# Kernel tuning notes

Hardware: AMD Instinct MI355X
Metric: run time of the kernel (lower is better)

## Reference

```python
import jax, jax.numpy as jnp
import numpy as np


def _update_cv(features, labels, ave, cov, amount, class_num):
    # Segment-reduce formulation of the onehot-expand update_CV.
    N, A = features.shape
    C = class_num
    counts = jax.ops.segment_sum(jnp.ones((N,), features.dtype), labels, num_segments=C)  # [C]
    sums = jax.ops.segment_sum(features, labels, num_segments=C)  # [C, A]
    denom = jnp.where(counts == 0, 1.0, counts)[:, None]  # Amount_CxA with zeros -> 1
    ave_CxA = sums / denom
    # var_temp: sum over samples of (x - mean_label)^2, divided by count
    diff = features - ave_CxA[labels]  # [N, A]
    sq = jax.ops.segment_sum(diff * diff, labels, num_segments=C)
    var_temp = sq / denom
    sum_weight = counts[:, None]  # [C,1] broadcast over A
    weight_CV = sum_weight / (sum_weight + amount[:, None])
    weight_CV = jnp.nan_to_num(weight_CV, nan=0.0)
    additional_CV = weight_CV * (1 - weight_CV) * (ave - ave_CxA) ** 2
    new_cov = cov * (1 - weight_CV) + var_temp * weight_CV + additional_CV
    new_ave = ave * (1 - weight_CV) + ave_CxA * weight_CV
    new_amount = amount + counts
    return new_ave, new_cov, new_amount


def _isda_aug(fc_weight, y, labels, cv_matrix, ratio):
    # sigma2[n,c] = ratio * sum_a (W[c,a] - W[labels[n],a])^2 * CV[labels[n],a]
    # = ratio * ( (W^2) @ cv_n - 2 W @ (w_n * cv_n) + sum_a w_n^2 cv_n )
    cv_n = cv_matrix[labels]              # [N, A]
    w_n = fc_weight[labels]               # [N, A]
    t1 = cv_n @ (fc_weight ** 2).T        # [N, C]
    t2 = (w_n * cv_n) @ fc_weight.T       # [N, C]
    t3 = jnp.sum(w_n * w_n * cv_n, axis=1, keepdims=True)  # [N, 1]
    sigma2 = ratio * (t1 - 2.0 * t2 + t3)
    return y + 0.5 * sigma2


def setup_inputs() -> dict:
    key = jax.random.key(0)
    k1, k2, k3, k4 = jax.random.split(key, 4)
    N, A, C = 512, 2048, 1000
    features = jax.random.normal(k1, (N, A), dtype=jnp.float32)
    labels = jax.random.randint(k2, (N,), 0, C)
    fc_weight = jax.random.normal(k3, (C, A), dtype=jnp.float32) * 0.02
    fc_bias = jax.random.normal(k4, (C,), dtype=jnp.float32) * 0.02
    return {
        "features": features,
        "labels": labels,
        "fc_weight": fc_weight,
        "fc_bias": fc_bias,
        "ave_state": jnp.zeros((C, A), jnp.float32),
        "cov_state": jnp.zeros((C, A), jnp.float32),
        "amount_state": jnp.zeros((C,), jnp.float32),
        "ratio": 1,
    }


def reference(features, labels, fc_weight, fc_bias, ave_state, cov_state, amount_state, ratio):
    C = fc_weight.shape[0]
    # model head: y = features @ W^T + b (features come from backbone; detached for CV)
    y = features @ fc_weight.T + fc_bias
    new_ave, new_cov, new_amount = _update_cv(
        jax.lax.stop_gradient(features), labels, ave_state, cov_state, amount_state, C)
    isda_y = _isda_aug(fc_weight, y, labels, jax.lax.stop_gradient(new_cov), ratio)
    log_probs = jax.nn.log_softmax(isda_y, axis=1)
    loss = -jnp.mean(jnp.take_along_axis(log_probs, labels[:, None], axis=1))
    return loss, y, new_ave, new_cov, new_amount
```

## Files before the change

kernel.cpp:

```cpp
#include <hip/hip_runtime.h>
#include <hip/hip_bf16.h>

typedef short v8s __attribute__((ext_vector_type(8)));
typedef float v4f __attribute__((ext_vector_type(4)));

#define KSPLIT 4

static __device__ __forceinline__ float ldv(const void* p, size_t i, int f32m) {
    if (f32m) return ((const float*)p)[i];
    return __bfloat162float(((const __hip_bfloat16*)p)[i]);
}
static __device__ __forceinline__ void stv(void* p, size_t i, float v, int f32m) {
    if (f32m) ((float*)p)[i] = v;
    else ((__hip_bfloat16*)p)[i] = __float2bfloat16(v);
}
static __device__ __forceinline__ unsigned short f2bu(float x) {
    __hip_bfloat16 h = __float2bfloat16(x);
    return *(unsigned short*)&h;
}
static __device__ __forceinline__ float bu2f(unsigned short u) {
    return __uint_as_float(((unsigned)u) << 16);
}

static __device__ __forceinline__ float decode_scalar(const void* p) {
    unsigned u = *(const unsigned*)p;
    unsigned e32 = (u >> 23) & 0xff;
    if (e32 >= 97 && e32 <= 160) return __uint_as_float(u);
    unsigned lo = u & 0xffffu;
    unsigned e16 = (lo >> 7) & 0xff;
    if ((u >> 16) == 0 && e16 >= 97 && e16 <= 160)
        return __uint_as_float(lo << 16);
    return (float)(int)u;
}

static __device__ __forceinline__ int block_sniff(const void* feat) {
    const __hip_bfloat16* p = (const __hip_bfloat16*)feat;
    float v = __bfloat162float(p[threadIdx.x & 255]);
    int bad = !(fabsf(v) < 1e10f);
    return __syncthreads_or(bad) ? 1 : 0;
}

__device__ __forceinline__ float wave_sum(float v) {
    #pragma unroll
    for (int o = 32; o > 0; o >>= 1) v += __shfl_down(v, o, 64);
    return v;
}
__device__ __forceinline__ float wave_max(float v) {
    #pragma unroll
    for (int o = 32; o > 0; o >>= 1) v = fmaxf(v, __shfl_down(v, o, 64));
    return v;
}

static __device__ __forceinline__ void ld16(unsigned short* lds, const unsigned short* g) {
    __builtin_amdgcn_global_load_lds(
        (const __attribute__((address_space(1))) unsigned int*)g,
        (__attribute__((address_space(3))) unsigned int*)lds,
        16, 0, 0);
}

__global__ __launch_bounds__(1024) void count_sort(
        const int* __restrict__ labels, int* __restrict__ counts,
        int* __restrict__ offs, int* __restrict__ rows, int Nn, int C) {
    __shared__ int h[1024];
    __shared__ int o[1024];
    __shared__ int cur[1024];
    int tid = threadIdx.x;
    h[tid] = 0;
    __syncthreads();
    for (int i = tid; i < Nn; i += 1024) atomicAdd(&h[labels[i]], 1);
    __syncthreads();
    o[tid] = h[tid];
    __syncthreads();
    for (int d = 1; d < 1024; d <<= 1) {
        int v = (tid >= d) ? o[tid - d] : 0;
        __syncthreads();
        o[tid] += v;
        __syncthreads();
    }
    int excl = o[tid] - h[tid];
    counts[tid] = h[tid];
    offs[tid] = excl;
    cur[tid] = excl;
    __syncthreads();
    for (int i = tid; i < Nn; i += 1024) {
        int pos = atomicAdd(&cur[labels[i]], 1);
        rows[pos] = i;
    }
}

__global__ __launch_bounds__(256) void prep(
        const void* __restrict__ feat, unsigned short* __restrict__ featb, int total) {
    int f32m = block_sniff(feat);
    int i = (blockIdx.x * 256 + threadIdx.x) * 8;
    if (i >= total) return;
    if (f32m) {
        const float* f = (const float*)feat + i;
        unsigned short r[8];
        #pragma unroll
        for (int u = 0; u < 8; ++u) r[u] = f2bu(f[u]);
        *(v8s*)(featb + i) = *(v8s*)r;
    } else {
        *(v8s*)(featb + i) = *(const v8s*)((const unsigned short*)feat + i);
    }
}

__global__ __launch_bounds__(256) void finalize_stats(
        const unsigned short* __restrict__ featb,
        const int* __restrict__ counts, const int* __restrict__ offs,
        const int* __restrict__ rows,
        const void* __restrict__ ave, const void* __restrict__ cov,
        const void* __restrict__ amount, const void* __restrict__ W,
        const void* __restrict__ feat,
        void* __restrict__ out, size_t off_ave, size_t off_cov, size_t off_amt,
        unsigned short* __restrict__ Wb, unsigned short* __restrict__ W2b,
        unsigned short* __restrict__ Cb, unsigned short* __restrict__ Gb,
        float* __restrict__ T3p, int A, int A8) {
    __shared__ float sb[4];
    int f32m = block_sniff(feat);
    int c = blockIdx.y;
    int a = blockIdx.x * 256 + threadIdx.x;
    size_t idx = (size_t)c * A + a;
    int cnti = counts[c];
    int start = offs[c];
    float s1 = 0.f, s2 = 0.f;
    for (int i = 0; i < cnti; ++i) {
        float x = bu2f(featb[(size_t)rows[start + i] * A + a]);
        s1 += x;
        s2 += x * x;
    }
    float cnt = (float)cnti;
    float denom = cnti > 0 ? cnt : 1.f;
    float mean = s1 / denom;
    float var = fmaxf((s2 - cnt * mean * mean) / denom, 0.f);
    float amt = ldv(amount, c, f32m);
    float tot = cnt + amt;
    float w = tot > 0.f ? (cnt / tot) : 0.f;
    float av = ldv(ave, idx, f32m);
    float cv = ldv(cov, idx, f32m);
    float d = av - mean;
    float ncv = cv * (1.f - w) + var * w + w * (1.f - w) * d * d;
    float nav = av * (1.f - w) + mean * w;
    stv(out, off_cov + idx, ncv, f32m);
    stv(out, off_ave + idx, nav, f32m);
    float wv = ldv(W, idx, f32m);
    Wb[idx] = f2bu(wv);
    W2b[idx] = f2bu(wv * wv);
    Cb[idx] = f2bu(ncv);
    Gb[idx] = f2bu(ncv * wv);
    if (a == 0) stv(out, off_amt + c, amt + cnt, f32m);
    float s = wave_sum(wv * wv * ncv);
    int lane = threadIdx.x & 63, wid = threadIdx.x >> 6;
    if (lane == 0) sb[wid] = s;
    __syncthreads();
    if (threadIdx.x == 0) T3p[(size_t)c * A8 + blockIdx.x] = sb[0] + sb[1] + sb[2] + sb[3];
}

__global__ __launch_bounds__(256) void triple_gemm_mfma(
        const unsigned short* __restrict__ featb,
        const unsigned short* __restrict__ Wb,
        const unsigned short* __restrict__ W2b,
        const unsigned short* __restrict__ Cb,
        const unsigned short* __restrict__ Gb,
        const int* __restrict__ labels,
        float* __restrict__ partY, float* __restrict__ partT1, float* __restrict__ partT2,
        int Cpad, int A, size_t NC) {
    __shared__ unsigned short sA[10240];
    __shared__ int sLab[64];
    int tid = threadIdx.x, wv = tid >> 6, lane = tid & 63;
    int n0 = blockIdx.y * 64, j0 = blockIdx.x * 64;
    int kslice = A / KSPLIT;
    int k0 = blockIdx.z * kslice;
    if (tid < 64) sLab[tid] = labels[n0 + tid];
    __syncthreads();

    int r = lane & 15, q = lane >> 4;
    int fr = wv * 16 + r;
    const unsigned short* pF = featb + (size_t)(n0 + fr) * A + k0 + q * 8;
    int lab = sLab[fr];
    const unsigned short* pC = Cb + (size_t)lab * A + k0 + q * 8;
    const unsigned short* pG = Gb + (size_t)lab * A + k0 + q * 8;
    const unsigned short* pW = Wb + (size_t)(j0 + fr) * A + k0 + q * 8;
    const unsigned short* pQ = W2b + (size_t)(j0 + fr) * A + k0 + q * 8;
    unsigned short* dF = &sA[0    + wv * 512];
    unsigned short* dC = &sA[2048 + wv * 512];
    unsigned short* dG = &sA[4096 + wv * 512];
    unsigned short* dW = &sA[6144 + wv * 512];
    unsigned short* dQ = &sA[8192 + wv * 512];

    v4f aY[4] = {{0,0,0,0},{0,0,0,0},{0,0,0,0},{0,0,0,0}};
    v4f aT1[4] = {{0,0,0,0},{0,0,0,0},{0,0,0,0},{0,0,0,0}};
    v4f aT2[4] = {{0,0,0,0},{0,0,0,0},{0,0,0,0},{0,0,0,0}};

    for (int kk = 0; kk < kslice; kk += 32) {
        ld16(dF, pF); ld16(dC, pC); ld16(dG, pG); ld16(dW, pW); ld16(dQ, pQ);
        pF += 32; pC += 32; pG += 32; pW += 32; pQ += 32;
        __syncthreads();
        v8s f = *(v8s*)&sA[0    + wv * 512 + lane * 8];
        v8s c = *(v8s*)&sA[2048 + wv * 512 + lane * 8];
        v8s g = *(v8s*)&sA[4096 + wv * 512 + lane * 8];
        #pragma unroll
        for (int t = 0; t < 4; ++t) {
            v8s w  = *(v8s*)&sA[6144 + t * 512 + lane * 8];
            v8s w2 = *(v8s*)&sA[8192 + t * 512 + lane * 8];
            aY[t]  = __builtin_amdgcn_mfma_f32_16x16x32_bf16(f, w,  aY[t],  0, 0, 0);
            aT1[t] = __builtin_amdgcn_mfma_f32_16x16x32_bf16(c, w2, aT1[t], 0, 0, 0);
            aT2[t] = __builtin_amdgcn_mfma_f32_16x16x32_bf16(g, w,  aT2[t], 0, 0, 0);
        }
        __syncthreads();
    }

    float* pY = partY + (size_t)blockIdx.z * NC;
    float* p1 = partT1 + (size_t)blockIdx.z * NC;
    float* p2 = partT2 + (size_t)blockIdx.z * NC;
    int quad = lane >> 4, colb = lane & 15;
    #pragma unroll
    for (int t = 0; t < 4; ++t) {
        int j = j0 + t * 16 + colb;
        #pragma unroll
        for (int rr = 0; rr < 4; ++rr) {
            int n = n0 + wv * 16 + quad * 4 + rr;
            size_t idx = (size_t)n * Cpad + j;
            pY[idx] = aY[t][rr];
            p1[idx] = aT1[t][rr];
            p2[idx] = aT2[t][rr];
        }
    }
}

__global__ __launch_bounds__(256) void epilogue_rowloss(
        const float* __restrict__ partY, const float* __restrict__ partT1,
        const float* __restrict__ partT2, const float* __restrict__ T3p,
        const void* __restrict__ bias, const void* __restrict__ feat,
        const int* __restrict__ labels,
        void* __restrict__ out, size_t off_y,
        float* __restrict__ rowloss,
        int C, int Cpad, int A8, const void* ratio_p, size_t NC) {
    __shared__ float sb[4];
    __shared__ float sM;
    __shared__ float sLabVal;
    int f32m = block_sniff(feat);
    int tid = threadIdx.x;
    int n = blockIdx.x;
    int lab = labels[n];
    float t3 = 0.f;
    for (int i = 0; i < A8; ++i) t3 += T3p[(size_t)lab * A8 + i];
    float ratio = decode_scalar(ratio_p);

    float vals[8];
    int nu = Cpad >> 8;
    float m = -3.4e38f;
    for (int u = 0; u < nu; ++u) {
        int j = u * 256 + tid;
        float v = -3.4e38f;
        if (j < C) {
            size_t idx = (size_t)n * Cpad + j;
            float y = 0.f, t1 = 0.f, t2 = 0.f;
            #pragma unroll
            for (int z = 0; z < KSPLIT; ++z) {
                y  += partY[z * NC + idx];
                t1 += partT1[z * NC + idx];
                t2 += partT2[z * NC + idx];
            }
            y += ldv(bias, j, f32m);
            stv(out, off_y + (size_t)n * C + j, y, f32m);
            v = y + 0.5f * ratio * (t1 - 2.f * t2 + t3);
            if (j == lab) sLabVal = v;
        }
        vals[u] = v;
        m = fmaxf(m, v);
    }
    m = wave_max(m);
    int lane = tid & 63, wid = tid >> 6;
    if (lane == 0) sb[wid] = m;
    __syncthreads();
    if (tid == 0) sM = fmaxf(fmaxf(sb[0], sb[1]), fmaxf(sb[2], sb[3]));
    __syncthreads();
    m = sM;
    float s = 0.f;
    for (int u = 0; u < nu; ++u) s += expf(vals[u] - m);
    __syncthreads();
    s = wave_sum(s);
    if (lane == 0) sb[wid] = s;
    __syncthreads();
    if (tid == 0)
        rowloss[n] = m + logf(sb[0] + sb[1] + sb[2] + sb[3]) - sLabVal;
}

__global__ __launch_bounds__(256) void final_loss(
        const float* __restrict__ rowloss, void* __restrict__ out,
        const void* __restrict__ feat, int Nn) {
    __shared__ float sb[4];
    int f32m = block_sniff(feat);
    float s = 0.f;
    for (int i = threadIdx.x; i < Nn; i += 256) s += rowloss[i];
    s = wave_sum(s);
    int lane = threadIdx.x & 63, wid = threadIdx.x >> 6;
    if (lane == 0) sb[wid] = s;
    __syncthreads();
    if (threadIdx.x == 0)
        stv(out, 0, (sb[0] + sb[1] + sb[2] + sb[3]) / (float)Nn, f32m);
}

extern "C" void kernel_launch(void* const* d_in, const int* in_sizes, int n_in,
                              void* d_out, int out_size, void* d_ws, size_t ws_size,
                              hipStream_t stream) {
    const void* feat   = d_in[0];
    const int*  labels = (const int*)d_in[1];
    const void* W      = d_in[2];
    const void* bias   = d_in[3];
    const void* ave    = d_in[4];
    const void* cov    = d_in[5];
    const void* amount = d_in[6];
    const void* ratiop = d_in[7];

    int NA = in_sizes[0];
    int Nn = in_sizes[1];
    int C  = in_sizes[3];
    int A  = NA / Nn;
    int CA = in_sizes[2];
    int Cpad = ((C + 255) / 256) * 256;
    int A8 = A / 256;
    size_t NC = (size_t)Nn * Cpad;

    size_t off_y   = 1;
    size_t off_ave = off_y + (size_t)Nn * C;
    size_t off_cov = off_ave + (size_t)CA;
    size_t off_amt = off_cov + (size_t)CA;

    char* ws = (char*)d_ws;
    int*   w_cnt  = (int*)ws;
    int*   w_off  = w_cnt + 1024;
    int*   w_rows = w_off + 1024;
    float* w_T3p  = (float*)(w_rows + 1024);
    float* w_rowls = w_T3p + 8192;
    float* w_partY  = w_rowls + 1024;
    float* w_partT1 = w_partY + KSPLIT * NC;
    float* w_partT2 = w_partT1 + KSPLIT * NC;
    unsigned short* w_featb = (unsigned short*)(w_partT2 + KSPLIT * NC);
    unsigned short* w_Wb    = w_featb + NA;
    unsigned short* w_W2b   = w_Wb + CA;
    unsigned short* w_Cb    = w_W2b + CA;
    unsigned short* w_Gb    = w_Cb + CA;

    count_sort<<<1, 1024, 0, stream>>>(labels, w_cnt, w_off, w_rows, Nn, C);
    prep<<<NA / 2048, 256, 0, stream>>>(feat, w_featb, NA);
    dim3 g2(A8, C);
    finalize_stats<<<g2, 256, 0, stream>>>(w_featb, w_cnt, w_off, w_rows,
                                           ave, cov, amount, W, feat,
                                           d_out, off_ave, off_cov, off_amt,
                                           w_Wb, w_W2b, w_Cb, w_Gb, w_T3p, A, A8);
    dim3 g3(Cpad / 64, Nn / 64, KSPLIT);
    triple_gemm_mfma<<<g3, 256, 0, stream>>>(w_featb, w_Wb, w_W2b, w_Cb, w_Gb,
                                             labels, w_partY, w_partT1, w_partT2,
                                             Cpad, A, NC);
    epilogue_rowloss<<<Nn, 256, 0, stream>>>(w_partY, w_partT1, w_partT2, w_T3p,
                                             bias, feat, labels, d_out, off_y,
                                             w_rowls, C, Cpad, A8, ratiop, NC);
    final_loss<<<1, 256, 0, stream>>>(w_rowls, d_out, feat, Nn);
}
```

Measured before the change: 140.0 us.

## Double-buffer GEMM LDS, fuse small kernels, vectorize stats, halve K-split

Several unrelated changes. The triple GEMM now double-buffers its LDS stages so the next k-tile loads while the current tile is in MFMA, and KSPLIT drops from 4 to 2, which shrinks the partial buffers but halves grid parallelism. count_sort and prep are merged into one launch, final_loss is folded into the epilogue through atomic accumulation plus a last-block counter, and finalize_stats handles two columns per thread with packed 32-bit loads and stores. Together these cut launch count and memory transactions, at the cost of fewer GEMM blocks and a nondeterministic float atomic sum for the loss.

```diff
diff --git a/kernel.cpp b/kernel.cpp
--- a/kernel.cpp
+++ b/kernel.cpp
@@ -4,7 +4,7 @@
 typedef short v8s __attribute__((ext_vector_type(8)));
 typedef float v4f __attribute__((ext_vector_type(4)));
 
-#define KSPLIT 4
+#define KSPLIT 2
 
 static __device__ __forceinline__ float ldv(const void* p, size_t i, int f32m) {
     if (f32m) return ((const float*)p)[i];
@@ -20,6 +20,16 @@
 }
 static __device__ __forceinline__ float bu2f(unsigned short u) {
     return __uint_as_float(((unsigned)u) << 16);
+}
+static __device__ __forceinline__ void ld2(const void* p, size_t i, int f32m, float* o) {
+    if (f32m) {
+        float2 v = *(const float2*)((const float*)p + i);
+        o[0] = v.x; o[1] = v.y;
+    } else {
+        unsigned u = *(const unsigned*)((const unsigned short*)p + i);
+        o[0] = bu2f((unsigned short)(u & 0xffffu));
+        o[1] = bu2f((unsigned short)(u >> 16));
+    }
 }
 
 static __device__ __forceinline__ float decode_scalar(const void* p) {
@@ -58,49 +68,51 @@
         16, 0, 0);
 }
 
-__global__ __launch_bounds__(1024) void count_sort(
+__global__ __launch_bounds__(1024) void sort_prep(
         const int* __restrict__ labels, int* __restrict__ counts,
-        int* __restrict__ offs, int* __restrict__ rows, int Nn, int C) {
+        int* __restrict__ offs, int* __restrict__ rows, int Nn, int C,
+        const void* __restrict__ feat, unsigned short* __restrict__ featb, int total,
+        float* __restrict__ lsum, int* __restrict__ lcnt) {
     __shared__ int h[1024];
     __shared__ int o[1024];
-    __shared__ int cur[1024];
+    __shared__ int cu[1024];
     int tid = threadIdx.x;
-    h[tid] = 0;
-    __syncthreads();
-    for (int i = tid; i < Nn; i += 1024) atomicAdd(&h[labels[i]], 1);
-    __syncthreads();
-    o[tid] = h[tid];
-    __syncthreads();
-    for (int d = 1; d < 1024; d <<= 1) {
-        int v = (tid >= d) ? o[tid - d] : 0;
+    if (blockIdx.x == 0) {
+        h[tid] = 0;
         __syncthreads();
-        o[tid] += v;
+        for (int i = tid; i < Nn; i += 1024) atomicAdd(&h[labels[i]], 1);
         __syncthreads();
-    }
-    int excl = o[tid] - h[tid];
-    counts[tid] = h[tid];
-    offs[tid] = excl;
-    cur[tid] = excl;
-    __syncthreads();
-    for (int i = tid; i < Nn; i += 1024) {
-        int pos = atomicAdd(&cur[labels[i]], 1);
-        rows[pos] = i;
-    }
-}
-
-__global__ __launch_bounds__(256) void prep(
-        const void* __restrict__ feat, unsigned short* __restrict__ featb, int total) {
-    int f32m = block_sniff(feat);
-    int i = (blockIdx.x * 256 + threadIdx.x) * 8;
-    if (i >= total) return;
-    if (f32m) {
-        const float* f = (const float*)feat + i;
-        unsigned short r[8];
-        #pragma unroll
-        for (int u = 0; u < 8; ++u) r[u] = f2bu(f[u]);
-        *(v8s*)(featb + i) = *(v8s*)r;
+        o[tid] = h[tid];
+        __syncthreads();
+        for (int d = 1; d < 1024; d <<= 1) {
+            int v = (tid >= d) ? o[tid - d] : 0;
+            __syncthreads();
+            o[tid] += v;
+            __syncthreads();
+        }
+        int excl = o[tid] - h[tid];
+        counts[tid] = h[tid];
+        offs[tid] = excl;
+        cu[tid] = excl;
+        __syncthreads();
+        for (int i = tid; i < Nn; i += 1024) {
+            int pos = atomicAdd(&cu[labels[i]], 1);
+            rows[pos] = i;
+        }
+        if (tid == 0) { *lsum = 0.f; *lcnt = 0; }
     } else {
-        *(v8s*)(featb + i) = *(const v8s*)((const unsigned short*)feat + i);
+        int f32m = block_sniff(feat);
+        int i = ((blockIdx.x - 1) * 1024 + tid) * 8;
+        if (i >= total) return;
+        if (f32m) {
+            const float* f = (const float*)feat + i;
+            unsigned short r[8];
+            #pragma unroll
+            for (int u = 0; u < 8; ++u) r[u] = f2bu(f[u]);
+            *(v8s*)(featb + i) = *(v8s*)r;
+        } else {
+            *(v8s*)(featb + i) = *(const v8s*)((const unsigned short*)feat + i);
+        }
     }
 }
 
@@ -118,37 +130,48 @@
     __shared__ float sb[4];
     int f32m = block_sniff(feat);
     int c = blockIdx.y;
-    int a = blockIdx.x * 256 + threadIdx.x;
+    int a = (blockIdx.x * 256 + threadIdx.x) * 2;
     size_t idx = (size_t)c * A + a;
     int cnti = counts[c];
     int start = offs[c];
-    float s1 = 0.f, s2 = 0.f;
+    float s1[2] = {0.f, 0.f}, s2[2] = {0.f, 0.f};
     for (int i = 0; i < cnti; ++i) {
-        float x = bu2f(featb[(size_t)rows[start + i] * A + a]);
-        s1 += x;
-        s2 += x * x;
+        unsigned u = *(const unsigned*)(featb + (size_t)rows[start + i] * A + a);
+        float x0 = bu2f((unsigned short)(u & 0xffffu));
+        float x1 = bu2f((unsigned short)(u >> 16));
+        s1[0] += x0; s2[0] += x0 * x0;
+        s1[1] += x1; s2[1] += x1 * x1;
     }
     float cnt = (float)cnti;
     float denom = cnti > 0 ? cnt : 1.f;
-    float mean = s1 / denom;
-    float var = fmaxf((s2 - cnt * mean * mean) / denom, 0.f);
     float amt = ldv(amount, c, f32m);
     float tot = cnt + amt;
     float w = tot > 0.f ? (cnt / tot) : 0.f;
-    float av = ldv(ave, idx, f32m);
-    float cv = ldv(cov, idx, f32m);
-    float d = av - mean;
-    float ncv = cv * (1.f - w) + var * w + w * (1.f - w) * d * d;
-    float nav = av * (1.f - w) + mean * w;
-    stv(out, off_cov + idx, ncv, f32m);
-    stv(out, off_ave + idx, nav, f32m);
-    float wv = ldv(W, idx, f32m);
-    Wb[idx] = f2bu(wv);
-    W2b[idx] = f2bu(wv * wv);
-    Cb[idx] = f2bu(ncv);
-    Gb[idx] = f2bu(ncv * wv);
+    float av[2], cv[2], wv[2];
+    ld2(ave, idx, f32m, av);
+    ld2(cov, idx, f32m, cv);
+    ld2(W, idx, f32m, wv);
+    unsigned short cb2[2], gb2[2];
+    float t3s = 0.f;
+    #pragma unroll
+    for (int k = 0; k < 2; ++k) {
+        float mean = s1[k] / denom;
+        float var = fmaxf((s2[k] - cnt * mean * mean) / denom, 0.f);
+        float d = av[k] - mean;
+        float ncv = cv[k] * (1.f - w) + var * w + w * (1.f - w) * d * d;
+        float nav = av[k] * (1.f - w) + mean * w;
+        stv(out, off_cov + idx + k, ncv, f32m);
+        stv(out, off_ave + idx + k, nav, f32m);
+        cb2[k] = f2bu(ncv);
+        gb2[k] = f2bu(ncv * wv[k]);
+        t3s += wv[k] * wv[k] * ncv;
+    }
+    *(unsigned*)(Wb + idx)  = (unsigned)f2bu(wv[0]) | ((unsigned)f2bu(wv[1]) << 16);
+    *(unsigned*)(W2b + idx) = (unsigned)f2bu(wv[0] * wv[0]) | ((unsigned)f2bu(wv[1] * wv[1]) << 16);
+    *(unsigned*)(Cb + idx)  = (unsigned)cb2[0] | ((unsigned)cb2[1] << 16);
+    *(unsigned*)(Gb + idx)  = (unsigned)gb2[0] | ((unsigned)gb2[1] << 16);
     if (a == 0) stv(out, off_amt + c, amt + cnt, f32m);
-    float s = wave_sum(wv * wv * ncv);
+    float s = wave_sum(t3s);
     int lane = threadIdx.x & 63, wid = threadIdx.x >> 6;
     if (lane == 0) sb[wid] = s;
     __syncthreads();
@@ -164,7 +187,7 @@
         const int* __restrict__ labels,
         float* __restrict__ partY, float* __restrict__ partT1, float* __restrict__ partT2,
         int Cpad, int A, size_t NC) {
-    __shared__ unsigned short sA[10240];
+    __shared__ unsigned short sA[2][10240];
     __shared__ int sLab[64];
     int tid = threadIdx.x, wv = tid >> 6, lane = tid & 63;
     int n0 = blockIdx.y * 64, j0 = blockIdx.x * 64;
@@ -181,33 +204,41 @@
     const unsigned short* pG = Gb + (size_t)lab * A + k0 + q * 8;
     const unsigned short* pW = Wb + (size_t)(j0 + fr) * A + k0 + q * 8;
     const unsigned short* pQ = W2b + (size_t)(j0 + fr) * A + k0 + q * 8;
-    unsigned short* dF = &sA[0    + wv * 512];
-    unsigned short* dC = &sA[2048 + wv * 512];
-    unsigned short* dG = &sA[4096 + wv * 512];
-    unsigned short* dW = &sA[6144 + wv * 512];
-    unsigned short* dQ = &sA[8192 + wv * 512];
 
     v4f aY[4] = {{0,0,0,0},{0,0,0,0},{0,0,0,0},{0,0,0,0}};
     v4f aT1[4] = {{0,0,0,0},{0,0,0,0},{0,0,0,0},{0,0,0,0}};
     v4f aT2[4] = {{0,0,0,0},{0,0,0,0},{0,0,0,0},{0,0,0,0}};
 
-    for (int kk = 0; kk < kslice; kk += 32) {
-        ld16(dF, pF); ld16(dC, pC); ld16(dG, pG); ld16(dW, pW); ld16(dQ, pQ);
-        pF += 32; pC += 32; pG += 32; pW += 32; pQ += 32;
-        __syncthreads();
-        v8s f = *(v8s*)&sA[0    + wv * 512 + lane * 8];
-        v8s c = *(v8s*)&sA[2048 + wv * 512 + lane * 8];
-        v8s g = *(v8s*)&sA[4096 + wv * 512 + lane * 8];
+    const int NIT = kslice / 32;
+
+    #define STAGE(b) do { \
+        ld16(&sA[b][0    + wv * 512], pF); \
+        ld16(&sA[b][2048 + wv * 512], pC); \
+        ld16(&sA[b][4096 + wv * 512], pG); \
+        ld16(&sA[b][6144 + wv * 512], pW); \
+        ld16(&sA[b][8192 + wv * 512], pQ); \
+        pF += 32; pC += 32; pG += 32; pW += 32; pQ += 32; } while (0)
+
+    STAGE(0);
+    asm volatile("s_waitcnt vmcnt(0)\n\ts_barrier" ::: "memory");
+
+    for (int it = 0; it < NIT; ++it) {
+        int bcur = it & 1;
+        if (it + 1 < NIT) STAGE(bcur ^ 1);
+        v8s f = *(v8s*)&sA[bcur][0    + wv * 512 + lane * 8];
+        v8s c = *(v8s*)&sA[bcur][2048 + wv * 512 + lane * 8];
+        v8s g = *(v8s*)&sA[bcur][4096 + wv * 512 + lane * 8];
         #pragma unroll
         for (int t = 0; t < 4; ++t) {
-            v8s w  = *(v8s*)&sA[6144 + t * 512 + lane * 8];
-            v8s w2 = *(v8s*)&sA[8192 + t * 512 + lane * 8];
+            v8s w  = *(v8s*)&sA[bcur][6144 + t * 512 + lane * 8];
+            v8s w2 = *(v8s*)&sA[bcur][8192 + t * 512 + lane * 8];
             aY[t]  = __builtin_amdgcn_mfma_f32_16x16x32_bf16(f, w,  aY[t],  0, 0, 0);
             aT1[t] = __builtin_amdgcn_mfma_f32_16x16x32_bf16(c, w2, aT1[t], 0, 0, 0);
             aT2[t] = __builtin_amdgcn_mfma_f32_16x16x32_bf16(g, w,  aT2[t], 0, 0, 0);
         }
-        __syncthreads();
-    }
+        asm volatile("s_waitcnt vmcnt(0)\n\ts_barrier" ::: "memory");
+    }
+    #undef STAGE
 
     float* pY = partY + (size_t)blockIdx.z * NC;
     float* p1 = partT1 + (size_t)blockIdx.z * NC;
@@ -233,8 +264,8 @@
         const void* __restrict__ bias, const void* __restrict__ feat,
         const int* __restrict__ labels,
         void* __restrict__ out, size_t off_y,
-        float* __restrict__ rowloss,
-        int C, int Cpad, int A8, const void* ratio_p, size_t NC) {
+        float* __restrict__ lsum, int* __restrict__ lcnt,
+        int C, int Cpad, int A8, const void* ratio_p, size_t NC, int Nn) {
     __shared__ float sb[4];
     __shared__ float sM;
     __shared__ float sLabVal;
@@ -282,23 +313,17 @@
     s = wave_sum(s);
     if (lane == 0) sb[wid] = s;
     __syncthreads();
-    if (tid == 0)
-        rowloss[n] = m + logf(sb[0] + sb[1] + sb[2] + sb[3]) - sLabVal;
-}
-
-__global__ __launch_bounds__(256) void final_loss(
-        const float* __restrict__ rowloss, void* __restrict__ out,
-        const void* __restrict__ feat, int Nn) {
-    __shared__ float sb[4];
-    int f32m = block_sniff(feat);
-    float s = 0.f;
-    for (int i = threadIdx.x; i < Nn; i += 256) s += rowloss[i];
-    s = wave_sum(s);
-    int lane = threadIdx.x & 63, wid = threadIdx.x >> 6;
-    if (lane == 0) sb[wid] = s;
-    __syncthreads();
-    if (threadIdx.x == 0)
-        stv(out, 0, (sb[0] + sb[1] + sb[2] + sb[3]) / (float)Nn, f32m);
+    if (tid == 0) {
+        float rl = m + logf(sb[0] + sb[1] + sb[2] + sb[3]) - sLabVal;
+        atomicAdd(lsum, rl);
+        __threadfence();
+        int old = atomicAdd(lcnt, 1);
+        if (old == Nn - 1) {
+            __threadfence();
+            float total = atomicAdd(lsum, 0.f);
+            stv(out, 0, total / (float)Nn, f32m);
+        }
+    }
 }
 
 extern "C" void kernel_launch(void* const* d_in, const int* in_sizes, int n_in,
@@ -319,7 +344,7 @@
     int A  = NA / Nn;
     int CA = in_sizes[2];
     int Cpad = ((C + 255) / 256) * 256;
-    int A8 = A / 256;
+    int A8 = A / 512;
     size_t NC = (size_t)Nn * Cpad;
 
     size_t off_y   = 1;
@@ -332,8 +357,9 @@
     int*   w_off  = w_cnt + 1024;
     int*   w_rows = w_off + 1024;
     float* w_T3p  = (float*)(w_rows + 1024);
-    float* w_rowls = w_T3p + 8192;
-    float* w_partY  = w_rowls + 1024;
+    float* w_lsum = w_T3p + 8192;
+    int*   w_lcnt = (int*)(w_lsum + 1);
+    float* w_partY  = w_lsum + 1024;
     float* w_partT1 = w_partY + KSPLIT * NC;
     float* w_partT2 = w_partT1 + KSPLIT * NC;
     unsigned short* w_featb = (unsigned short*)(w_partT2 + KSPLIT * NC);
@@ -342,9 +368,10 @@
     unsigned short* w_Cb    = w_W2b + CA;
     unsigned short* w_Gb    = w_Cb + CA;
 
-    count_sort<<<1, 1024, 0, stream>>>(labels, w_cnt, w_off, w_rows, Nn, C);
-    prep<<<NA / 2048, 256, 0, stream>>>(feat, w_featb, NA);
-    dim3 g2(A8, C);
+    int prep_blocks = NA / 8192;
+    sort_prep<<<1 + prep_blocks, 1024, 0, stream>>>(
+        labels, w_cnt, w_off, w_rows, Nn, C, feat, w_featb, NA, w_lsum, w_lcnt);
+    dim3 g2(A / 512, C);
     finalize_stats<<<g2, 256, 0, stream>>>(w_featb, w_cnt, w_off, w_rows,
                                            ave, cov, amount, W, feat,
                                            d_out, off_ave, off_cov, off_amt,
@@ -355,6 +382,6 @@
                                              Cpad, A, NC);
     epilogue_rowloss<<<Nn, 256, 0, stream>>>(w_partY, w_partT1, w_partT2, w_T3p,
                                              bias, feat, labels, d_out, off_y,
-                                             w_rowls, C, Cpad, A8, ratiop, NC);
-    final_loss<<<1, 256, 0, stream>>>(w_rowls, d_out, feat, Nn);
-}
+                                             w_lsum, w_lcnt,
+                                             C, Cpad, A8, ratiop, NC, Nn);
+}
```

Measured after the change: 157.4 us. 1.12x slower.
